# Performance work log

Hardware: AMD Instinct MI355X
Metric: run time of the kernel (lower is better)

Reference implementation:

```python
import jax, jax.numpy as jnp
import numpy as np

N, C, T, V, K = 64, 64, 300, 25, 3
EPS = 1e-5


def setup_inputs() -> dict:
    key = jax.random.key(0)
    ks = jax.random.split(key, 4)
    x = jax.random.normal(ks[0], (N, C, T, V), dtype=jnp.float32)
    A = jax.random.uniform(ks[1], (K, V, V), dtype=jnp.float32)
    # per-subset 1x1 conv weights: W[k] maps C_in -> C_out, plus bias b[k]
    W = jax.random.normal(ks[2], (K, C, C), dtype=jnp.float32) * (1.0 / np.sqrt(C))
    b = jax.random.normal(ks[3], (K, C), dtype=jnp.float32) * 0.01
    gamma = jnp.ones((C,), dtype=jnp.float32)
    beta = jnp.zeros((C,), dtype=jnp.float32)
    return {"x": x, "A": A, "W": W, "b": b, "gamma": gamma, "beta": beta}


def reference(x, A, W, b, gamma, beta):
    # y = sum_k conv1x1_k( einsum('nctv,vw->nctw', x, A[k]) )
    # conv1x1 over (C,T,V) with kernel 1 == channel matmul; fuse subsets via one einsum.
    y = jnp.einsum('nctv,kvw,koc->notw', x, A, W)
    y = y + jnp.sum(b, axis=0)[None, :, None, None]
    # BatchNorm2d in training mode: batch statistics over (N, T, V) per channel
    mean = jnp.mean(y, axis=(0, 2, 3), keepdims=True)
    var = jnp.mean(jnp.square(y - mean), axis=(0, 2, 3), keepdims=True)
    y = gamma[None, :, None, None] * (y - mean) * jax.lax.rsqrt(var + EPS) + beta[None, :, None, None]
    # residual (in_channels == out_channels -> identity) + relu
    return jax.nn.relu(y + x)
```

## Files before the change

kernel.cpp:

```cpp
#include <hip/hip_runtime.h>
#include <hip/hip_bf16.h>

#define N_ 64
#define C_ 64
#define T_ 300
#define V_ 25
#define K_ 3
#define TT 12
#define NTILE 25
#define NBLK 1600
#define XROW 384
#define WP 72
#define ATP 40
#define NTHR 512
#define EPS_ 1e-5f

typedef __bf16 bf16_t;
typedef __bf16 bf16x4 __attribute__((ext_vector_type(4)));
typedef __bf16 bf16x8 __attribute__((ext_vector_type(8)));
typedef float f32x4 __attribute__((ext_vector_type(4)));
typedef float f32x4u __attribute__((ext_vector_type(4), aligned(4)));

static __device__ __forceinline__ bf16_t tobf(float f) { return (bf16_t)f; }
static __device__ __forceinline__ int emask(int c) { return ((c & 3) << 3) | ((c & 8) << 2); }

union SmemU {
  struct { bf16_t W[3 * 64 * WP]; bf16_t At[3 * 32 * ATP]; } wa;
  bf16_t xs[64 * XROW];
};

struct Frags {
  bf16x8 wfrag[6];
  bf16x8 afrag[3][2];
  int fK[4], fS5[4];
  float bs[4];
  int obase;
};

static __device__ __forceinline__ void stage_wa(
    const float* __restrict__ A, const float* __restrict__ W, SmemU& sm, int tid) {
  for (int m = tid; m < 3072; m += NTHR) {
    f32x4 v4 = *(reinterpret_cast<const f32x4*>(W) + m);
    int f = m << 2;
    int k = f >> 12, o = (f >> 6) & 63, c = f & 63;
    bf16x4 h;
    h[0] = tobf(v4[0]); h[1] = tobf(v4[1]); h[2] = tobf(v4[2]); h[3] = tobf(v4[3]);
    *reinterpret_cast<bf16x4*>(&sm.wa.W[(k * 64 + o) * WP + c]) = h;
  }
  for (int i = tid; i < 3072; i += NTHR) {
    int k = i >> 10, r = i & 1023, w = r >> 5, v = r & 31;
    float val = (v < V_ && w < V_) ? A[k * 625 + v * 25 + w] : 0.f;
    sm.wa.At[(k * 32 + w) * ATP + v] = tobf(val);
  }
}

static __device__ __forceinline__ void read_frags(
    const SmemU& sm, const float* __restrict__ b, int ob, int l15, int lg, Frags& F) {
  const int o = ob * 16 + l15;
  #pragma unroll
  for (int k = 0; k < 3; ++k)
    #pragma unroll
    for (int ch = 0; ch < 2; ++ch)
      F.wfrag[k * 2 + ch] =
          *reinterpret_cast<const bf16x8*>(&sm.wa.W[(k * 64 + o) * WP + ch * 32 + lg * 8]);
  #pragma unroll
  for (int k = 0; k < 3; ++k)
    #pragma unroll
    for (int wh = 0; wh < 2; ++wh)
      F.afrag[k][wh] =
          *reinterpret_cast<const bf16x8*>(&sm.wa.At[(k * 32 + wh * 16 + l15) * ATP + lg * 8]);
  const int crow = 8 * (l15 >> 2) + (l15 & 3);
  #pragma unroll
  for (int q = 0; q < 4; ++q) {
    int c = ((q >> 1) * 32) + ((q & 1) * 4) + crow;
    int em = emask(c);
    F.fK[q] = c * XROW + ((lg * 8) ^ (em & 24));
    F.fS5[q] = em & 32;
  }
  F.obase = ob * 16 + lg * 4;
  #pragma unroll
  for (int r = 0; r < 4; ++r)
    F.bs[r] = b[F.obase + r] + b[64 + F.obase + r] + b[128 + F.obase + r];
}

static __device__ __forceinline__ void stage_x(
    const float* __restrict__ x, SmemU& sm, int n, int t0, int tid) {
  const int c = tid >> 3, vb = tid & 7;
  const int em = emask(c);
  const float* xr = x + (size_t)n * 480000 + (size_t)c * 7500 + (size_t)t0 * 25;
  bf16_t* xsr = &sm.xs[c * XROW];
  #pragma unroll
  for (int t = 0; t < TT; ++t) {
    bf16x4 h;
    if (vb < 6) {
      f32x4u v4 = *reinterpret_cast<const f32x4u*>(xr + t * 25 + vb * 4);
      h[0] = tobf(v4[0]); h[1] = tobf(v4[1]); h[2] = tobf(v4[2]); h[3] = tobf(v4[3]);
    } else if (vb == 6) {
      float s = xr[t * 25 + 24];
      h[0] = tobf(s); h[1] = tobf(0.f); h[2] = tobf(0.f); h[3] = tobf(0.f);
    } else {
      h[0] = tobf(0.f); h[1] = tobf(0.f); h[2] = tobf(0.f); h[3] = tobf(0.f);
    }
    *reinterpret_cast<bf16x4*>(&xsr[(((t << 5) + vb * 4) ^ em)]) = h;
  }
}

static __device__ __forceinline__ void compute_wh(
    const bf16x8* xf, const Frags& F, int wh, f32x4& acc0, f32x4& acc1) {
  acc0 = f32x4{0.f, 0.f, 0.f, 0.f};
  acc1 = f32x4{0.f, 0.f, 0.f, 0.f};
  #pragma unroll
  for (int k = 0; k < 3; ++k) {
    #pragma unroll
    for (int ch = 0; ch < 2; ++ch) {
      f32x4 zero = {0.f, 0.f, 0.f, 0.f};
      f32x4 dP = __builtin_amdgcn_mfma_f32_16x16x32_bf16(xf[ch * 2 + 0], F.afrag[k][wh], zero, 0, 0, 0);
      f32x4 dQ = __builtin_amdgcn_mfma_f32_16x16x32_bf16(xf[ch * 2 + 1], F.afrag[k][wh], zero, 0, 0, 0);
      bf16x8 zf;
      zf[0] = tobf(dP[0]); zf[1] = tobf(dP[1]); zf[2] = tobf(dP[2]); zf[3] = tobf(dP[3]);
      zf[4] = tobf(dQ[0]); zf[5] = tobf(dQ[1]); zf[6] = tobf(dQ[2]); zf[7] = tobf(dQ[3]);
      if (ch == 0)
        acc0 = __builtin_amdgcn_mfma_f32_16x16x32_bf16(F.wfrag[k * 2 + ch], zf, acc0, 0, 0, 0);
      else
        acc1 = __builtin_amdgcn_mfma_f32_16x16x32_bf16(F.wfrag[k * 2 + ch], zf, acc1, 0, 0, 0);
    }
  }
}

__global__ __launch_bounds__(NTHR, 4) void k1_compute(
    const float* __restrict__ x, const float* __restrict__ A,
    const float* __restrict__ W, const float* __restrict__ b,
    float* __restrict__ y, float* __restrict__ part) {
  __shared__ __align__(16) SmemU sm;
  __shared__ float stats2[2][2][64];

  const int bid = (blockIdx.x & 7) * (NBLK / 8) + (blockIdx.x >> 3);
  const int n = bid / NTILE;
  const int t0 = (bid - n * NTILE) * TT;
  const int tid = threadIdx.x;
  const int lane = tid & 63;
  const int wv = tid >> 6;
  const int ob = wv & 3;
  const int th = wv >> 2;
  const int l15 = lane & 15;
  const int lg = lane >> 4;

  stage_wa(A, W, sm, tid);
  __syncthreads();
  Frags F;
  read_frags(sm, b, ob, l15, lg, F);
  __syncthreads();
  stage_x(x, sm, n, t0, tid);
  __syncthreads();

  float lsum[4] = {0.f, 0.f, 0.f, 0.f}, lsq[4] = {0.f, 0.f, 0.f, 0.f};
  const int w_lo = l15, w_hi = 16 + l15;
  float* yb = y + (size_t)n * 480000 + (size_t)t0 * 25;

  #pragma unroll 2
  for (int tl = 0; tl < 6; ++tl) {
    const int t = th * 6 + tl;
    bf16x8 xf[4];
    #pragma unroll
    for (int q = 0; q < 4; ++q)
      xf[q] = *reinterpret_cast<const bf16x8*>(sm.xs + F.fK[q] + ((t << 5) ^ F.fS5[q]));
    #pragma unroll
    for (int wh = 0; wh < 2; ++wh) {
      f32x4 acc0, acc1;
      compute_wh(xf, F, wh, acc0, acc1);
      const int w = wh ? w_hi : w_lo;
      if (w < V_) {
        #pragma unroll
        for (int r = 0; r < 4; ++r) {
          float val = acc0[r] + acc1[r] + F.bs[r];
          lsum[r] += val;
          lsq[r] += val * val;
          yb[(size_t)(F.obase + r) * 7500 + t * 25 + w] = val;
        }
      }
    }
  }

  #pragma unroll
  for (int d = 1; d < 16; d <<= 1) {
    #pragma unroll
    for (int r = 0; r < 4; ++r) {
      lsum[r] += __shfl_xor(lsum[r], d);
      lsq[r]  += __shfl_xor(lsq[r], d);
    }
  }
  if (l15 == 0) {
    #pragma unroll
    for (int r = 0; r < 4; ++r) {
      stats2[0][th][F.obase + r] = lsum[r];
      stats2[1][th][F.obase + r] = lsq[r];
    }
  }
  __syncthreads();
  if (tid < 128)
    part[(size_t)bid * 128 + tid] =
        stats2[tid >> 6][0][tid & 63] + stats2[tid >> 6][1][tid & 63];
}

__global__ __launch_bounds__(256) void k2_stats(
    const float* __restrict__ part,
    const float* __restrict__ gamma, const float* __restrict__ beta,
    float* __restrict__ ss) {
  const int o = blockIdx.x;
  const int tid = threadIdx.x;
  double s = 0.0, q = 0.0;
  for (int i = tid; i < NBLK; i += 256) {
    s += (double)part[(size_t)i * 128 + o];
    q += (double)part[(size_t)i * 128 + 64 + o];
  }
  __shared__ double sd[256], qd[256];
  sd[tid] = s; qd[tid] = q;
  __syncthreads();
  for (int step = 128; step > 0; step >>= 1) {
    if (tid < step) { sd[tid] += sd[tid + step]; qd[tid] += qd[tid + step]; }
    __syncthreads();
  }
  if (tid == 0) {
    const double cnt = 480000.0;
    double mean = sd[0] / cnt;
    double var = qd[0] / cnt - mean * mean;
    float inv = rsqrtf((float)var + EPS_);
    float sc = gamma[o] * inv;
    float sh = beta[o] - (float)mean * sc;
    ss[2 * o] = sc;
    ss[2 * o + 1] = sh;
  }
}

__global__ __launch_bounds__(256) void k3_finish(
    const float* __restrict__ x, const float* __restrict__ ss,
    float* __restrict__ y) {
  const int p = blockIdx.x;
  const int c = p & 63;
  const float sc = ss[2 * c];
  const float sh = ss[2 * c + 1];
  const float4* xv = reinterpret_cast<const float4*>(x + (size_t)p * 7500);
  float4* yv = reinterpret_cast<float4*>(y + (size_t)p * 7500);
  for (int i = threadIdx.x; i < 1875; i += 256) {
    float4 a = yv[i];
    float4 b4 = xv[i];
    float4 o;
    o.x = fmaxf(sc * a.x + sh + b4.x, 0.f);
    o.y = fmaxf(sc * a.y + sh + b4.y, 0.f);
    o.z = fmaxf(sc * a.z + sh + b4.z, 0.f);
    o.w = fmaxf(sc * a.w + sh + b4.w, 0.f);
    yv[i] = o;
  }
}

extern "C" void kernel_launch(void* const* d_in, const int* in_sizes, int n_in,
                              void* d_out, int out_size, void* d_ws, size_t ws_size,
                              hipStream_t stream) {
  const float* x     = (const float*)d_in[0];
  const float* A     = (const float*)d_in[1];
  const float* W     = (const float*)d_in[2];
  const float* b     = (const float*)d_in[3];
  const float* gamma = (const float*)d_in[4];
  const float* beta  = (const float*)d_in[5];
  float* y = (float*)d_out;

  float* part = (float*)d_ws;
  float* ss   = part + (size_t)NBLK * 128;

  k1_compute<<<NBLK, NTHR, 0, stream>>>(x, A, W, b, y, part);
  k2_stats<<<64, 256, 0, stream>>>(part, gamma, beta, ss);
  k3_finish<<<4096, 256, 0, stream>>>(x, ss, y);
}
```

Measured before the change: 145.4 us.

## Recompute graph conv in apply pass instead of storing and rereading y

The first kernel now only computes BatchNorm statistics and no longer writes the intermediate y. The final kernel recomputes the MFMA graph convolution per tile and applies scale, shift, residual and ReLU in one pass, reading the residual from the bf16 copy staged in shared memory. Each block also handles two tiles, and a throwaway prefetch loop touches the x tiles early. This trades the y write plus its later read for a second full compute pass and an extra read of x. It also uses a bf16-rounded residual, which may cost accuracy.

After: 169.8 us. +16.8%, slower.

```diff
diff --git a/kernel.cpp b/kernel.cpp
--- a/kernel.cpp
+++ b/kernel.cpp
@@ -9,6 +9,7 @@
 #define TT 12
 #define NTILE 25
 #define NBLK 1600
+#define NPERS 800
 #define XROW 384
 #define WP 72
 #define ATP 40
@@ -81,6 +82,24 @@
   #pragma unroll
   for (int r = 0; r < 4; ++r)
     F.bs[r] = b[F.obase + r] + b[64 + F.obase + r] + b[128 + F.obase + r];
+}
+
+static __device__ __forceinline__ void prestream2(
+    const float* __restrict__ x, int bid, int tid) {
+  float sink = 0.f;
+  const int c = tid >> 3, q = tid & 7;
+  #pragma unroll
+  for (int i = 0; i < 2; ++i) {
+    const int tile = bid * 2 + i;
+    const int n = tile / NTILE;
+    const int t0 = (tile - n * NTILE) * TT;
+    const float* tb = x + (size_t)n * 480000 + (size_t)c * 7500 + (size_t)t0 * 25;
+    for (int j = q; j < 75; j += 8) {
+      f32x4 v = *reinterpret_cast<const f32x4*>(tb + 4 * j);
+      sink += v[0] + v[1] + v[2] + v[3];
+    }
+  }
+  asm volatile("" :: "v"(sink));
 }
 
 static __device__ __forceinline__ void stage_x(
@@ -127,16 +146,14 @@
   }
 }
 
-__global__ __launch_bounds__(NTHR, 4) void k1_compute(
+__global__ __launch_bounds__(NTHR, 4) void k1_stats(
     const float* __restrict__ x, const float* __restrict__ A,
     const float* __restrict__ W, const float* __restrict__ b,
-    float* __restrict__ y, float* __restrict__ part) {
+    float* __restrict__ part) {
   __shared__ __align__(16) SmemU sm;
   __shared__ float stats2[2][2][64];
 
-  const int bid = (blockIdx.x & 7) * (NBLK / 8) + (blockIdx.x >> 3);
-  const int n = bid / NTILE;
-  const int t0 = (bid - n * NTILE) * TT;
+  const int bid = blockIdx.x;
   const int tid = threadIdx.x;
   const int lane = tid & 63;
   const int wv = tid >> 6;
@@ -146,39 +163,46 @@
   const int lg = lane >> 4;
 
   stage_wa(A, W, sm, tid);
+  prestream2(x, bid, tid);
   __syncthreads();
   Frags F;
   read_frags(sm, b, ob, l15, lg, F);
   __syncthreads();
-  stage_x(x, sm, n, t0, tid);
-  __syncthreads();
 
   float lsum[4] = {0.f, 0.f, 0.f, 0.f}, lsq[4] = {0.f, 0.f, 0.f, 0.f};
-  const int w_lo = l15, w_hi = 16 + l15;
-  float* yb = y + (size_t)n * 480000 + (size_t)t0 * 25;
-
-  #pragma unroll 2
-  for (int tl = 0; tl < 6; ++tl) {
-    const int t = th * 6 + tl;
-    bf16x8 xf[4];
-    #pragma unroll
-    for (int q = 0; q < 4; ++q)
-      xf[q] = *reinterpret_cast<const bf16x8*>(sm.xs + F.fK[q] + ((t << 5) ^ F.fS5[q]));
-    #pragma unroll
-    for (int wh = 0; wh < 2; ++wh) {
-      f32x4 acc0, acc1;
-      compute_wh(xf, F, wh, acc0, acc1);
-      const int w = wh ? w_hi : w_lo;
-      if (w < V_) {
-        #pragma unroll
-        for (int r = 0; r < 4; ++r) {
-          float val = acc0[r] + acc1[r] + F.bs[r];
-          lsum[r] += val;
-          lsq[r] += val * val;
-          yb[(size_t)(F.obase + r) * 7500 + t * 25 + w] = val;
+
+  #pragma unroll
+  for (int i = 0; i < 2; ++i) {
+    const int tile = bid * 2 + i;
+    const int n = tile / NTILE;
+    const int t0 = (tile - n * NTILE) * TT;
+
+    stage_x(x, sm, n, t0, tid);
+    __syncthreads();
+
+    #pragma unroll 2
+    for (int tl = 0; tl < 6; ++tl) {
+      const int t = th * 6 + tl;
+      bf16x8 xf[4];
+      #pragma unroll
+      for (int q = 0; q < 4; ++q)
+        xf[q] = *reinterpret_cast<const bf16x8*>(sm.xs + F.fK[q] + ((t << 5) ^ F.fS5[q]));
+      #pragma unroll
+      for (int wh = 0; wh < 2; ++wh) {
+        f32x4 acc0, acc1;
+        compute_wh(xf, F, wh, acc0, acc1);
+        const int w = wh ? 16 + l15 : l15;
+        if (w < V_) {
+          #pragma unroll
+          for (int r = 0; r < 4; ++r) {
+            float val = acc0[r] + acc1[r] + F.bs[r];
+            lsum[r] += val;
+            lsq[r] += val * val;
+          }
         }
       }
     }
+    __syncthreads();
   }
 
   #pragma unroll
@@ -209,7 +233,7 @@
   const int o = blockIdx.x;
   const int tid = threadIdx.x;
   double s = 0.0, q = 0.0;
-  for (int i = tid; i < NBLK; i += 256) {
+  for (int i = tid; i < NPERS; i += 256) {
     s += (double)part[(size_t)i * 128 + o];
     q += (double)part[(size_t)i * 128 + 64 + o];
   }
@@ -232,24 +256,69 @@
   }
 }
 
-__global__ __launch_bounds__(256) void k3_finish(
-    const float* __restrict__ x, const float* __restrict__ ss,
-    float* __restrict__ y) {
-  const int p = blockIdx.x;
-  const int c = p & 63;
-  const float sc = ss[2 * c];
-  const float sh = ss[2 * c + 1];
-  const float4* xv = reinterpret_cast<const float4*>(x + (size_t)p * 7500);
-  float4* yv = reinterpret_cast<float4*>(y + (size_t)p * 7500);
-  for (int i = threadIdx.x; i < 1875; i += 256) {
-    float4 a = yv[i];
-    float4 b4 = xv[i];
-    float4 o;
-    o.x = fmaxf(sc * a.x + sh + b4.x, 0.f);
-    o.y = fmaxf(sc * a.y + sh + b4.y, 0.f);
-    o.z = fmaxf(sc * a.z + sh + b4.z, 0.f);
-    o.w = fmaxf(sc * a.w + sh + b4.w, 0.f);
-    yv[i] = o;
+__global__ __launch_bounds__(NTHR, 4) void k3_apply(
+    const float* __restrict__ x, const float* __restrict__ A,
+    const float* __restrict__ W, const float* __restrict__ b,
+    const float* __restrict__ ss, float* __restrict__ out) {
+  __shared__ __align__(16) SmemU sm;
+
+  const int bid = blockIdx.x;
+  const int tid = threadIdx.x;
+  const int lane = tid & 63;
+  const int wv = tid >> 6;
+  const int ob = wv & 3;
+  const int th = wv >> 2;
+  const int l15 = lane & 15;
+  const int lg = lane >> 4;
+
+  stage_wa(A, W, sm, tid);
+  __syncthreads();
+  Frags F;
+  read_frags(sm, b, ob, l15, lg, F);
+
+  float sc[4], sh[4];
+  #pragma unroll
+  for (int r = 0; r < 4; ++r) {
+    sc[r] = ss[2 * (F.obase + r)];
+    sh[r] = ss[2 * (F.obase + r) + 1];
+  }
+  __syncthreads();
+
+  #pragma unroll
+  for (int i = 0; i < 2; ++i) {
+    const int tile = bid * 2 + i;
+    const int n = tile / NTILE;
+    const int t0 = (tile - n * NTILE) * TT;
+
+    stage_x(x, sm, n, t0, tid);
+    __syncthreads();
+
+    float* obp = out + (size_t)n * 480000 + (size_t)t0 * 25;
+
+    #pragma unroll 2
+    for (int tl = 0; tl < 6; ++tl) {
+      const int t = th * 6 + tl;
+      bf16x8 xf[4];
+      #pragma unroll
+      for (int q = 0; q < 4; ++q)
+        xf[q] = *reinterpret_cast<const bf16x8*>(sm.xs + F.fK[q] + ((t << 5) ^ F.fS5[q]));
+      #pragma unroll
+      for (int wh = 0; wh < 2; ++wh) {
+        f32x4 acc0, acc1;
+        compute_wh(xf, F, wh, acc0, acc1);
+        const int w = wh ? 16 + l15 : l15;
+        if (w < V_) {
+          #pragma unroll
+          for (int r = 0; r < 4; ++r) {
+            const int o = F.obase + r;
+            float val = acc0[r] + acc1[r] + F.bs[r];
+            float xr = (float)sm.xs[o * XROW + (((t << 5) + w) ^ emask(o))];
+            obp[(size_t)o * 7500 + t * 25 + w] = fmaxf(sc[r] * val + sh[r] + xr, 0.f);
+          }
+        }
+      }
+    }
+    __syncthreads();
   }
 }
 
@@ -262,12 +331,12 @@
   const float* b     = (const float*)d_in[3];
   const float* gamma = (const float*)d_in[4];
   const float* beta  = (const float*)d_in[5];
-  float* y = (float*)d_out;
+  float* out = (float*)d_out;
 
   float* part = (float*)d_ws;
-  float* ss   = part + (size_t)NBLK * 128;
-
-  k1_compute<<<NBLK, NTHR, 0, stream>>>(x, A, W, b, y, part);
+  float* ss   = part + (size_t)NPERS * 128;
+
+  k1_stats<<<NPERS, NTHR, 0, stream>>>(x, A, W, b, part);
   k2_stats<<<64, 256, 0, stream>>>(part, gamma, beta, ss);
-  k3_finish<<<4096, 256, 0, stream>>>(x, ss, y);
-}
+  k3_apply<<<NPERS, NTHR, 0, stream>>>(x, A, W, b, ss, out);
+}
```

## Process two tiles per block and prefetch the next tile's x into cache

Applied to the files above, without the earlier changes.

Halves the grid so each block handles two consecutive time tiles, amortizing the W/A staging and fragment setup across both. It also issues scattered touch loads of the upcoming tile's x rows (first tile during weight staging, second during compute) so they are cache-resident when staged. The dummy loads are kept alive with an empty asm sink. This drops the XCD-interleaved block remapping and halves the partial-stats count, which reduces parallelism and may hurt load balance across CUs.

Result: slower. 153.8 us (+5.7%).

```diff
diff --git a/kernel.cpp b/kernel.cpp
--- a/kernel.cpp
+++ b/kernel.cpp
@@ -9,6 +9,7 @@
 #define TT 12
 #define NTILE 25
 #define NBLK 1600
+#define NPERS 800
 #define XROW 384
 #define WP 72
 #define ATP 40
@@ -81,6 +82,20 @@
   #pragma unroll
   for (int r = 0; r < 4; ++r)
     F.bs[r] = b[F.obase + r] + b[64 + F.obase + r] + b[128 + F.obase + r];
+}
+
+static __device__ __forceinline__ void touch_issue(
+    const float* __restrict__ x, int tile, int tid, float* tv) {
+  const int n = tile / NTILE;
+  const int t0 = (tile - n * NTILE) * TT;
+  const float* base = x + (size_t)n * 480000 + (size_t)t0 * 25;
+  #pragma unroll
+  for (int j = 0; j < 3; ++j) {
+    int idx = tid + (j << 9);
+    int c = idx / 19;
+    int li = idx - c * 19;
+    tv[j] = (c < 64) ? base[(size_t)c * 7500 + li * 16] : 0.f;
+  }
 }
 
 static __device__ __forceinline__ void stage_x(
@@ -134,9 +149,7 @@
   __shared__ __align__(16) SmemU sm;
   __shared__ float stats2[2][2][64];
 
-  const int bid = (blockIdx.x & 7) * (NBLK / 8) + (blockIdx.x >> 3);
-  const int n = bid / NTILE;
-  const int t0 = (bid - n * NTILE) * TT;
+  const int bid = blockIdx.x;
   const int tid = threadIdx.x;
   const int lane = tid & 63;
   const int wv = tid >> 6;
@@ -145,41 +158,61 @@
   const int l15 = lane & 15;
   const int lg = lane >> 4;
 
-  stage_wa(A, W, sm, tid);
+  float sink = 0.f;
+  {
+    float tv0[3];
+    touch_issue(x, bid * 2, tid, tv0);
+    stage_wa(A, W, sm, tid);
+    sink += tv0[0] + tv0[1] + tv0[2];
+  }
   __syncthreads();
   Frags F;
   read_frags(sm, b, ob, l15, lg, F);
   __syncthreads();
-  stage_x(x, sm, n, t0, tid);
-  __syncthreads();
 
   float lsum[4] = {0.f, 0.f, 0.f, 0.f}, lsq[4] = {0.f, 0.f, 0.f, 0.f};
-  const int w_lo = l15, w_hi = 16 + l15;
-  float* yb = y + (size_t)n * 480000 + (size_t)t0 * 25;
-
-  #pragma unroll 2
-  for (int tl = 0; tl < 6; ++tl) {
-    const int t = th * 6 + tl;
-    bf16x8 xf[4];
-    #pragma unroll
-    for (int q = 0; q < 4; ++q)
-      xf[q] = *reinterpret_cast<const bf16x8*>(sm.xs + F.fK[q] + ((t << 5) ^ F.fS5[q]));
-    #pragma unroll
-    for (int wh = 0; wh < 2; ++wh) {
-      f32x4 acc0, acc1;
-      compute_wh(xf, F, wh, acc0, acc1);
-      const int w = wh ? w_hi : w_lo;
-      if (w < V_) {
-        #pragma unroll
-        for (int r = 0; r < 4; ++r) {
-          float val = acc0[r] + acc1[r] + F.bs[r];
-          lsum[r] += val;
-          lsq[r] += val * val;
-          yb[(size_t)(F.obase + r) * 7500 + t * 25 + w] = val;
+
+  #pragma unroll
+  for (int i = 0; i < 2; ++i) {
+    const int tile = bid * 2 + i;
+    const int n = tile / NTILE;
+    const int t0 = (tile - n * NTILE) * TT;
+
+    stage_x(x, sm, n, t0, tid);
+    __syncthreads();
+
+    float tv[3] = {0.f, 0.f, 0.f};
+    if (i == 0) touch_issue(x, tile + 1, tid, tv);
+
+    float* yb = y + (size_t)n * 480000 + (size_t)t0 * 25;
+
+    #pragma unroll 2
+    for (int tl = 0; tl < 6; ++tl) {
+      const int t = th * 6 + tl;
+      bf16x8 xf[4];
+      #pragma unroll
+      for (int q = 0; q < 4; ++q)
+        xf[q] = *reinterpret_cast<const bf16x8*>(sm.xs + F.fK[q] + ((t << 5) ^ F.fS5[q]));
+      #pragma unroll
+      for (int wh = 0; wh < 2; ++wh) {
+        f32x4 acc0, acc1;
+        compute_wh(xf, F, wh, acc0, acc1);
+        const int w = wh ? 16 + l15 : l15;
+        if (w < V_) {
+          #pragma unroll
+          for (int r = 0; r < 4; ++r) {
+            float val = acc0[r] + acc1[r] + F.bs[r];
+            lsum[r] += val;
+            lsq[r] += val * val;
+            yb[(size_t)(F.obase + r) * 7500 + t * 25 + w] = val;
+          }
         }
       }
     }
-  }
+    sink += tv[0] + tv[1] + tv[2];
+    __syncthreads();
+  }
+  asm volatile("" :: "v"(sink));
 
   #pragma unroll
   for (int d = 1; d < 16; d <<= 1) {
@@ -209,7 +242,7 @@
   const int o = blockIdx.x;
   const int tid = threadIdx.x;
   double s = 0.0, q = 0.0;
-  for (int i = tid; i < NBLK; i += 256) {
+  for (int i = tid; i < NPERS; i += 256) {
     s += (double)part[(size_t)i * 128 + o];
     q += (double)part[(size_t)i * 128 + 64 + o];
   }
@@ -265,9 +298,9 @@
   float* y = (float*)d_out;
 
   float* part = (float*)d_ws;
-  float* ss   = part + (size_t)NBLK * 128;
-
-  k1_compute<<<NBLK, NTHR, 0, stream>>>(x, A, W, b, y, part);
+  float* ss   = part + (size_t)NPERS * 128;
+
+  k1_compute<<<NPERS, NTHR, 0, stream>>>(x, A, W, b, y, part);
   k2_stats<<<64, 256, 0, stream>>>(part, gamma, beta, ss);
   k3_finish<<<4096, 256, 0, stream>>>(x, ss, y);
 }
```
